# Optimization experiments

Measured on AMD Instinct MI355X. Metric: run time of the kernel, lower is better.

The kernel has to match this reference:

```python
import jax, jax.numpy as jnp
import numpy as np

N_WAY = 5
K_SHOT = 5
TEMPERATURE = 1.0
NEG = -1e9  # emulates 'column does not exist' for pad columns beyond umask_length
EPS = 1e-12  # matches torch F.normalize eps


def _l2n(x, axis):
    n = jnp.sqrt(jnp.sum(x * x, axis=axis, keepdims=True))
    return x / jnp.maximum(n, EPS)


def setup_inputs() -> dict:
    key = jax.random.key(0)
    k1, k2, k3, k4, k5 = jax.random.split(key, 5)
    b, c, h, w = 4, 64, 5, 5
    q, u = 75, 100
    support_xf = jax.random.normal(k1, (b, N_WAY * K_SHOT, c, h, w), jnp.float32)
    query_xf = jax.random.normal(k2, (b, q, c, h, w), jnp.float32)
    unlabeled_xf = jax.random.normal(k3, (b, u, c, h, w), jnp.float32)
    support_y = jax.random.randint(k4, (b, N_WAY * K_SHOT), 0, N_WAY)
    query_y = jax.random.randint(k5, (b, q), 0, N_WAY)
    return {"support_xf": support_xf, "support_y": support_y, "query_xf": query_xf,
            "query_y": query_y, "unlabeled_xf": unlabeled_xf}


def _forward(support_xf, query_xf, unlabeled_xf, query_y):
    b, q, c, h, w = query_xf.shape
    M_s = K_SHOT * h * w
    unl = unlabeled_xf.reshape(b, -1, c, h, w)
    u = unl.shape[1]
    M_u = u * h * w
    # pooled unlabeled local descriptors, flattened in (u, h, w) order -> [b, c, M_u]
    unl_feat = unl.transpose(0, 2, 1, 3, 4).reshape(b, c, M_u)
    # support -> [b, n_way, c, k_shot*h*w]
    sup = support_xf.reshape(b, N_WAY, K_SHOT, c, h, w).transpose(0, 1, 3, 2, 4, 5).reshape(b, N_WAY, c, M_s)
    # cosine similarity unlabeled -> support: [b, n_way, M_u, M_s]
    u2s = jnp.einsum('bwcn,bcm->bwmn', _l2n(sup, 2), _l2n(unl_feat, 1))
    pool = u2s.transpose(0, 2, 1, 3).reshape(b, M_u, N_WAY * M_s)
    s_nearest = jnp.argmax(pool, axis=1)          # per support loc: nearest unlabeled loc
    u_nearest = jnp.argmax(pool, axis=2)          # per unlabeled loc: nearest support loc
    mutual = jnp.take_along_axis(s_nearest, u_nearest, axis=1) == jnp.arange(M_u)[None, :]  # [b, M_u]
    # class with max similarity per unlabeled location
    cls = jnp.argmax(jnp.max(u2s, axis=-1), axis=1)  # [b, M_u]
    umask = jax.nn.one_hot(cls, N_WAY, dtype=jnp.float32).transpose(0, 2, 1) \
            * mutual[:, None, :].astype(jnp.float32)  # [b, n_way, M_u]
    counts = umask.sum(-1)                          # [b, n_way]
    L = counts.max()                                # umask_length (traced)
    # stream compaction via stable argsort of the 0/1 mask (preserves original order)
    order = jnp.argsort(-umask, axis=-1)            # jnp.argsort is stable
    pts = unl_feat.transpose(0, 2, 1)               # [b, M_u, c]
    gath = jnp.take_along_axis(pts[:, None, :, :], order[..., None], axis=2)  # [b, n_way, M_u, c]
    valid = (jnp.arange(M_u)[None, None, :] < counts[:, :, None]).astype(jnp.float32)
    comp = gath * valid[..., None]                  # rows beyond count are zeros (as in torch)
    s_cat = jnp.concatenate([sup, comp.transpose(0, 1, 3, 2)], axis=-1)  # [b, n_way, c, M_s+M_u]
    M_tot = M_s + M_u
    qn = _l2n(query_xf.reshape(b, q, c, h * w), 2)
    scn = _l2n(s_cat, 2)
    sim = jnp.einsum('bqcm,bwcn->bqwmn', qn, scn)   # [b, q, n_way, M_q, M_tot]
    sim = (sim + 1.0) * 0.5                          # FourLayer_64F branch
    # columns beyond umask_length don't exist in the torch dense tensor -> exclude from maxes
    pad = jnp.arange(M_tot)[None, None, None, None, :] >= (M_s + L)
    sim = jnp.where(pad, NEG, sim)
    M_q = h * w
    qm = sim.transpose(0, 1, 3, 2, 4).reshape(b, q, M_q, N_WAY * M_tot)
    support_nearest = jnp.argmax(qm, axis=2)        # [b, q, n_way*M_tot]
    query_nearest = jnp.argmax(qm, axis=3)          # [b, q, M_q]
    g = jnp.take_along_axis(support_nearest, query_nearest, axis=2)
    q_mask = (g == jnp.arange(M_q)[None, None, :]).astype(sim.dtype)  # mutual NN mask
    query_value = (jnp.max(sim, axis=-1) * q_mask[:, :, None, :]).sum(-1)  # [b, q, n_way]
    logits = query_value.reshape(b * q, N_WAY) / TEMPERATURE
    y = query_y.reshape(b * q)
    logp = jax.nn.log_softmax(logits, axis=-1)
    loss = -jnp.take_along_axis(logp, y[:, None], axis=1).mean()
    return loss


def reference(support_xf, support_y, query_xf, query_y, unlabeled_xf):
    return _forward(support_xf, query_xf, unlabeled_xf, query_y)
```

## Files before the change

### kernel.cpp

```cpp
#include <hip/hip_runtime.h>

#define NEGINF (-1e30f)

constexpr size_t OF_UNL  = 0;
constexpr size_t OF_SUP  = OF_UNL  + (size_t)4*2500*64;
constexpr size_t OF_SUPT = OF_SUP  + (size_t)4*5*125*64;
constexpr size_t OF_QT   = OF_SUPT + (size_t)4*5*64*128;
constexpr size_t OF_ROWV = OF_QT   + (size_t)300*28*64;
constexpr size_t OF_ROWI = OF_ROWV + (size_t)4*5*8*2500;
constexpr size_t OF_CVI  = OF_ROWI + (size_t)4*5*8*2500;
constexpr size_t OF_CMP  = OF_CVI  + (size_t)4*5*125*20*2;
constexpr size_t OF_CNT  = OF_CMP  + (size_t)4*5*2500;
constexpr size_t OF_UNEAR= OF_CNT  + 20;
constexpr size_t OF_SNEAR= OF_UNEAR+ 10000;
constexpr size_t OF_BV   = OF_SNEAR+ 2500;
constexpr size_t OF_BP   = OF_BV   + 37500;
constexpr size_t OF_AMX  = OF_BP   + 37500;

typedef __attribute__((ext_vector_type(4)))  float f4s;
typedef __attribute__((ext_vector_type(16))) float f16s;

__global__ __launch_bounds__(256) void knorm(
    const float* __restrict__ sup, const float* __restrict__ qry,
    const float* __restrict__ unl,
    float* __restrict__ unl_n, float* __restrict__ sup_n,
    float* __restrict__ supT, float* __restrict__ qt)
{
    int gid = blockIdx.x * 256 + threadIdx.x;
    if (gid >= 320000) {
        int t = gid - 320000;
        if (t < 14400) {
            int bq = t / 48, r = t % 48;
            int row = 25 + r / 16, ch = r % 16;
            *(float4*)(qt + ((size_t)bq * 28 + row) * 64 + ch * 4) =
                make_float4(0.f, 0.f, 0.f, 0.f);
        }
        return;
    }
    int loc = gid >> 4;
    int sub = gid & 15;

    const float* src;
    float* dst1; int dstr1;
    float* dst2 = nullptr;

    if (loc < 10000) {
        int b = loc / 2500, m = loc % 2500;
        int u = m / 25, hw = m % 25;
        src  = unl + ((size_t)(b*100 + u) * 64) * 25 + hw;
        dst1 = unl_n + (size_t)loc * 64; dstr1 = 1;
    } else if (loc < 12500) {
        int idx = loc - 10000;
        int b = idx / 625, r = idx % 625;
        int w = r / 125,  n = r % 125;
        int shot = n / 25, hw = n % 25;
        src  = sup + ((size_t)(b*25 + w*5 + shot) * 64) * 25 + hw;
        dst1 = sup_n + (size_t)idx * 64; dstr1 = 1;
        dst2 = supT + ((size_t)(b*5 + w) * 64) * 128 + n;
    } else {
        int idx = loc - 12500;
        int bq = idx / 25, mq = idx % 25;
        src  = qry + ((size_t)bq * 64) * 25 + mq;
        dst1 = qt + ((size_t)bq * 28 + mq) * 64; dstr1 = 1;
    }

    float v[4]; float ss = 0.f;
    int c0 = sub * 4;
#pragma unroll
    for (int j = 0; j < 4; ++j) { v[j] = src[(size_t)(c0 + j) * 25]; ss += v[j] * v[j]; }
#pragma unroll
    for (int msk = 1; msk < 16; msk <<= 1) ss += __shfl_xor(ss, msk);
    float sc = 1.f / fmaxf(sqrtf(ss), 1e-12f);
#pragma unroll
    for (int j = 0; j < 4; ++j) {
        float o = v[j] * sc;
        dst1[(size_t)(c0 + j) * dstr1] = o;
        if (dst2) dst2[(size_t)(c0 + j) * 128] = o;
    }
}

#define KB2(C) { \
    f16s s0, s1; \
    asm volatile("s_load_dwordx16 %0, %[b], %c[o0]\n\t" \
                 "s_load_dwordx16 %1, %[b], %c[o1]\n\t" \
                 "s_waitcnt lgkmcnt(0)" \
                 : "=s"(s0), "=s"(s1) \
                 : [b]"s"(sbp), [o0]"i"((C)*512), [o1]"i"((C)*512+512)); \
    float2 uv = *(const float2*)&uls[ml * 66 + (C)]; \
    acc[0]  = fmaf(uv.x, s0[0],  fmaf(uv.y, s1[0],  acc[0])); \
    acc[1]  = fmaf(uv.x, s0[1],  fmaf(uv.y, s1[1],  acc[1])); \
    acc[2]  = fmaf(uv.x, s0[2],  fmaf(uv.y, s1[2],  acc[2])); \
    acc[3]  = fmaf(uv.x, s0[3],  fmaf(uv.y, s1[3],  acc[3])); \
    acc[4]  = fmaf(uv.x, s0[4],  fmaf(uv.y, s1[4],  acc[4])); \
    acc[5]  = fmaf(uv.x, s0[5],  fmaf(uv.y, s1[5],  acc[5])); \
    acc[6]  = fmaf(uv.x, s0[6],  fmaf(uv.y, s1[6],  acc[6])); \
    acc[7]  = fmaf(uv.x, s0[7],  fmaf(uv.y, s1[7],  acc[7])); \
    acc[8]  = fmaf(uv.x, s0[8],  fmaf(uv.y, s1[8],  acc[8])); \
    acc[9]  = fmaf(uv.x, s0[9],  fmaf(uv.y, s1[9],  acc[9])); \
    acc[10] = fmaf(uv.x, s0[10], fmaf(uv.y, s1[10], acc[10])); \
    acc[11] = fmaf(uv.x, s0[11], fmaf(uv.y, s1[11], acc[11])); \
    acc[12] = fmaf(uv.x, s0[12], fmaf(uv.y, s1[12], acc[12])); \
    acc[13] = fmaf(uv.x, s0[13], fmaf(uv.y, s1[13], acc[13])); \
    acc[14] = fmaf(uv.x, s0[14], fmaf(uv.y, s1[14], acc[14])); \
    acc[15] = fmaf(uv.x, s0[15], fmaf(uv.y, s1[15], acc[15])); }
#define KB8(C) KB2(C) KB2((C)+2) KB2((C)+4) KB2((C)+6)

__global__ __launch_bounds__(256) void kb(
    const float* __restrict__ unl_n, const float* __restrict__ supT,
    float* __restrict__ rowv, int* __restrict__ rowi, float* __restrict__ colvi)
{
    int bid = blockIdx.x;
    int nc = bid & 3;
    int mb = (bid >> 2) % 20;
    int bw = bid / 80;
    int b  = bw / 5;
    int tid = threadIdx.x;
    int lane = tid & 63, wv = tid >> 6;

    __shared__ float uls[128 * 66];
    __shared__ float sv_[4][32];
    __shared__ int   si_[4][32];

    int m0 = mb * 128;
    int n0 = nc * 32;

    for (int i = tid; i < 128 * 16; i += 256) {
        int row = i >> 4, c4 = (i & 15) * 4;
        int m = m0 + row;
        float4 x = make_float4(0.f, 0.f, 0.f, 0.f);
        if (m < 2500) x = *(const float4*)(unl_n + ((size_t)(b * 2500 + m)) * 64 + c4);
        *(float2*)&uls[row * 66 + c4]     = make_float2(x.x, x.y);
        *(float2*)&uls[row * 66 + c4 + 2] = make_float2(x.z, x.w);
    }
    __syncthreads();

    int ml = tid & 127;
    int m  = m0 + ml;
    int nh = tid >> 7;
    int nbase = nh * 16;
    int nbu = __builtin_amdgcn_readfirstlane(nbase);
    int nn_total = (125 - n0) < 32 ? (125 - n0) : 32;
    const float* sbp = supT + ((size_t)bw * 64) * 128 + n0 + nbu;

    float acc[16];
#pragma unroll
    for (int j = 0; j < 16; ++j) acc[j] = 0.f;

    KB8(0)  KB8(8)  KB8(16) KB8(24)
    KB8(32) KB8(40) KB8(48) KB8(56)

    int nnloc = nn_total - nbase;
    nnloc = nnloc < 0 ? 0 : (nnloc > 16 ? 16 : nnloc);
    float rbv = NEGINF; int rbi = 0;
    for (int j = 0; j < nnloc; ++j)
        if (acc[j] > rbv) { rbv = acc[j]; rbi = n0 + nbase + j; }
    if (m < 2500) {
        int ck = nc * 2 + nh;
        rowv[((size_t)bw * 8 + ck) * 2500 + m] = rbv;
        rowi[((size_t)bw * 8 + ck) * 2500 + m] = rbi;
    }

#pragma unroll
    for (int j = 0; j < 16; ++j) {
        float v = (m < 2500 && (nbase + j) < nn_total) ? acc[j] : NEGINF;
        float vm = v;
#pragma unroll
        for (int s2 = 1; s2 < 64; s2 <<= 1) vm = fmaxf(vm, __shfl_xor(vm, s2));
        unsigned long long msk = __ballot(v == vm);
        int first = __ffsll((unsigned long long)msk) - 1;
        if (lane == 0) { sv_[wv][nbase + j] = vm; si_[wv][nbase + j] = m0 + (wv & 1) * 64 + first; }
    }
    __syncthreads();
    if (tid < nn_total) {
        int w0 = (tid < 16) ? 0 : 2;
        float v = sv_[w0][tid];     int vi = si_[w0][tid];
        float v2 = sv_[w0 + 1][tid]; int i2 = si_[w0 + 1][tid];
        if (v2 > v || (v2 == v && i2 < vi)) { v = v2; vi = i2; }
        float* cv = colvi + ((((size_t)bw) * 125 + (n0 + tid)) * 20 + mb) * 2;
        cv[0] = v; ((int*)cv)[1] = vi;
    }
}

__global__ __launch_bounds__(64) void kmerge(
    const float* __restrict__ rowv, const int* __restrict__ rowi,
    const float* __restrict__ colvi,
    int* __restrict__ unear, int* __restrict__ snear)
{
    int it = blockIdx.x * 64 + threadIdx.x;
    if (it < 10000) {
        int b = it / 2500, m = it % 2500;
        float bv = NEGINF; int bi = 0;
#pragma unroll
        for (int w = 0; w < 5; ++w) {
#pragma unroll
            for (int ck = 0; ck < 8; ++ck) {
                size_t o = (((size_t)(b * 5 + w)) * 8 + ck) * 2500 + m;
                float v = rowv[o];
                if (v > bv) { bv = v; bi = w * 125 + rowi[o]; }
            }
        }
        unear[it] = bi;
    } else if (it < 12500) {
        int idx = it - 10000;
        const float* p = colvi + (size_t)idx * 40;
        float bv = NEGINF; int bi = 0x7fffffff;
        for (int mb2 = 0; mb2 < 20; ++mb2) {
            float v = p[mb2 * 2]; int vi = ((const int*)p)[mb2 * 2 + 1];
            if (v > bv || (v == bv && vi < bi)) { bv = v; bi = vi; }
        }
        snear[idx] = bi;
    }
}

__global__ __launch_bounds__(256) void kcmp(
    const int* __restrict__ unear, const int* __restrict__ snear,
    int* __restrict__ cmp, int* __restrict__ cntg)
{
    int p = blockIdx.x;
    int b = p / 5, way = p % 5;
    int tid = threadIdx.x, lane = tid & 63, wv = tid >> 6;
    __shared__ unsigned long long masks[40];
    __shared__ int base[40];

    for (int ch = wv; ch < 40; ch += 4) {
        int m = ch * 64 + lane;
        bool ok = false;
        if (m < 2500) {
            int un = unear[b * 2500 + m];
            ok = (un / 125 == way) && (snear[b * 625 + un] == m);
        }
        unsigned long long msk = __ballot(ok ? 1 : 0);
        if (lane == 0) masks[ch] = msk;
    }
    __syncthreads();
    if (tid == 0) {
        int s = 0;
        for (int ch = 0; ch < 40; ++ch) { base[ch] = s; s += __popcll(masks[ch]); }
        cntg[p] = s;
    }
    __syncthreads();
    for (int ch = wv; ch < 40; ch += 4) {
        unsigned long long msk = masks[ch];
        if ((msk >> lane) & 1ull) {
            int pre = __popcll(msk & ((1ull << lane) - 1ull));
            cmp[(size_t)p * 2500 + base[ch] + pre] = ch * 64 + lane;
        }
    }
}

#define QLOAD(CG, Q0,Q1,Q2,Q3,Q4,Q5,Q6) \
  asm volatile( \
    "s_load_dwordx4 %0, %[b], %c[o0]\n\t" \
    "s_load_dwordx4 %1, %[b], %c[o1]\n\t" \
    "s_load_dwordx4 %2, %[b], %c[o2]\n\t" \
    "s_load_dwordx4 %3, %[b], %c[o3]\n\t" \
    "s_load_dwordx4 %4, %[b], %c[o4]\n\t" \
    "s_load_dwordx4 %5, %[b], %c[o5]\n\t" \
    "s_load_dwordx4 %6, %[b], %c[o6]\n\t" \
    "s_waitcnt lgkmcnt(0)" \
    : "=s"(Q0), "=s"(Q1), "=s"(Q2), "=s"(Q3), "=s"(Q4), "=s"(Q5), "=s"(Q6) \
    : [b]"s"(qbp), \
      [o0]"i"((CG)*16 + 0*256), [o1]"i"((CG)*16 + 1*256), \
      [o2]"i"((CG)*16 + 2*256), [o3]"i"((CG)*16 + 3*256), \
      [o4]"i"((CG)*16 + 4*256), [o5]"i"((CG)*16 + 5*256), \
      [o6]"i"((CG)*16 + 6*256))

#define CGSTEP(CG) { \
    f4s q0,q1,q2,q3,q4,q5,q6; \
    QLOAD(CG, q0,q1,q2,q3,q4,q5,q6); \
    float4 cl = *(const float4*)&cls[lane * 68 + (CG) * 4]; \
    acc[0]=fmaf(q0.x,cl.x,fmaf(q0.y,cl.y,fmaf(q0.z,cl.z,fmaf(q0.w,cl.w,acc[0])))); \
    acc[1]=fmaf(q1.x,cl.x,fmaf(q1.y,cl.y,fmaf(q1.z,cl.z,fmaf(q1.w,cl.w,acc[1])))); \
    acc[2]=fmaf(q2.x,cl.x,fmaf(q2.y,cl.y,fmaf(q2.z,cl.z,fmaf(q2.w,cl.w,acc[2])))); \
    acc[3]=fmaf(q3.x,cl.x,fmaf(q3.y,cl.y,fmaf(q3.z,cl.z,fmaf(q3.w,cl.w,acc[3])))); \
    acc[4]=fmaf(q4.x,cl.x,fmaf(q4.y,cl.y,fmaf(q4.z,cl.z,fmaf(q4.w,cl.w,acc[4])))); \
    acc[5]=fmaf(q5.x,cl.x,fmaf(q5.y,cl.y,fmaf(q5.z,cl.z,fmaf(q5.w,cl.w,acc[5])))); \
    acc[6]=fmaf(q6.x,cl.x,fmaf(q6.y,cl.y,fmaf(q6.z,cl.z,fmaf(q6.w,cl.w,acc[6])))); }

__global__ __launch_bounds__(256) void kc1(
    const float* __restrict__ qt, const float* __restrict__ sup_n,
    const float* __restrict__ unl_n, const int* __restrict__ cmp,
    const int* __restrict__ cntg,
    float* __restrict__ bvg, int* __restrict__ bpg,
    unsigned char* __restrict__ amaxg)
{
    int bid = blockIdx.x;
    int w = bid % 5, bq = bid / 5;
    int b = bq / 75;
    int tid = threadIdx.x;
    int lane = tid & 63;
    int wvu = __builtin_amdgcn_readfirstlane(tid >> 6);
    int pbw = b * 5 + w;

    int L = 0;
#pragma unroll
    for (int i = 0; i < 20; ++i) { int v = cntg[i]; L = L > v ? L : v; }
    int cntw = 0, wb = 0;
#pragma unroll
    for (int w2 = 0; w2 < 5; ++w2) {
        int c2 = cntg[b * 5 + w2];
        if (w2 < w) wb += 125 + c2;
        if (w2 == w) cntw = c2;
    }
    int cw = 125 + cntw;

    __shared__ float cls[64 * 68];
    __shared__ float amxv[4][64];
    __shared__ int   amxg_[4][64];
    __shared__ float redv[25];
    __shared__ int   redn[25];

    const float* qbp = qt + ((size_t)bq * 28 + wvu * 7) * 64;

    float rv[7]; int rn[7];
#pragma unroll
    for (int j = 0; j < 7; ++j) { rv[j] = NEGINF; rn[j] = 0x7fffffff; }

    int nb = (cw + 63) >> 6;

    for (int b4 = 0; b4 < nb; ++b4) {
        if (b4 > 0 && tid < 64) {
            int n = (b4 - 1) * 64 + tid;
            if (n < cw) {
                float v = amxv[0][tid]; int g = amxg_[0][tid];
#pragma unroll
                for (int g2 = 1; g2 < 4; ++g2)
                    if (amxv[g2][tid] > v) { v = amxv[g2][tid]; g = amxg_[g2][tid]; }
                amaxg[(size_t)bq * 3200 + (wb + n)] = (unsigned char)g;
            }
        }
#pragma unroll
        for (int k = 0; k < 4; ++k) {
            int i = tid + k * 256;
            int row = i >> 4, ch = i & 15;
            int n = b4 * 64 + row;
            float4 x = make_float4(0.f, 0.f, 0.f, 0.f);
            if (n < cw) {
                const float* cp;
                if (n < 125) cp = sup_n + (((size_t)pbw) * 125 + n) * 64;
                else { int m = cmp[((size_t)pbw) * 2500 + (n - 125)];
                       cp = unl_n + ((size_t)(b * 2500 + m)) * 64; }
                x = *(const float4*)(cp + ch * 4);
            }
            *(float4*)&cls[row * 68 + ch * 4] = x;
        }
        __syncthreads();

        float acc[7];
#pragma unroll
        for (int j = 0; j < 7; ++j) acc[j] = 0.f;

        CGSTEP(0);  CGSTEP(1);  CGSTEP(2);  CGSTEP(3);
        CGSTEP(4);  CGSTEP(5);  CGSTEP(6);  CGSTEP(7);
        CGSTEP(8);  CGSTEP(9);  CGSTEP(10); CGSTEP(11);
        CGSTEP(12); CGSTEP(13); CGSTEP(14); CGSTEP(15);

        bool colvalid = (b4 * 64 + lane) < cw;
        float cmax = NEGINF; int cam = 0;
#pragma unroll
        for (int j = 0; j < 7; ++j) {
            int mq = wvu * 7 + j;
            float s = (acc[j] + 1.0f) * 0.5f;
            float sm = (colvalid && mq < 25) ? s : NEGINF;
            if (sm > cmax) { cmax = sm; cam = mq; }
            float vm = sm;
#pragma unroll
            for (int t = 1; t < 64; t <<= 1) vm = fmaxf(vm, __shfl_xor(vm, t));
            unsigned long long msk = __ballot(sm == vm);
            int first = __ffsll(msk) - 1;
            if (vm > rv[j]) { rv[j] = vm; rn[j] = b4 * 64 + first; }
        }
        amxv[wvu][lane] = cmax; amxg_[wvu][lane] = cam;
        __syncthreads();
    }

    if (tid < 64) {
        int n = (nb - 1) * 64 + tid;
        if (n < cw) {
            float v = amxv[0][tid]; int g = amxg_[0][tid];
#pragma unroll
            for (int g2 = 1; g2 < 4; ++g2)
                if (amxv[g2][tid] > v) { v = amxv[g2][tid]; g = amxg_[g2][tid]; }
            amaxg[(size_t)bq * 3200 + (wb + n)] = (unsigned char)g;
        }
    }
    if (lane == 0) {
#pragma unroll
        for (int j = 0; j < 7; ++j) {
            int mq = wvu * 7 + j;
            if (mq < 25) { redv[mq] = rv[j]; redn[mq] = rn[j]; }
        }
    }
    __syncthreads();

    if (tid < 25) {
        float v = redv[tid]; int nn = redn[tid];
        int p = ((w * 2625 + nn) << 12) | (wb + nn);
        if (L > cntw) {
            int pp = ((w * 2625 + 125 + cntw) << 12) | 0xFFF;
            if (0.5f > v || (0.5f == v && pp < p)) { v = 0.5f; p = pp; }
        }
        size_t o = ((size_t)bq * 5 + w) * 25 + tid;
        bvg[o] = v; bpg[o] = p;
    }
}

__global__ __launch_bounds__(64) void kce(
    const float* __restrict__ bvg, const int* __restrict__ bpg,
    const unsigned char* __restrict__ amaxg, const int* __restrict__ qy,
    float* __restrict__ out)
{
    int bq = blockIdx.x;
    int tid = threadIdx.x;
    __shared__ float qmask[25];
    __shared__ float lg[5];
    if (tid < 25) {
        float v = NEGINF; int p = 0x7fffffff;
#pragma unroll
        for (int w = 0; w < 5; ++w) {
            size_t o = ((size_t)bq * 5 + w) * 25 + tid;
            float v2 = bvg[o]; int p2 = bpg[o];
            if (v2 > v || (v2 == v && p2 < p)) { v = v2; p = p2; }
        }
        int pos = p & 0xFFF;
        int g = (pos == 0xFFF) ? 0 : (int)amaxg[(size_t)bq * 3200 + pos];
        qmask[tid] = (g == tid) ? 1.0f : 0.0f;
    }
    __syncthreads();
    if (tid < 5) {
        float s = 0.f;
#pragma unroll
        for (int mq = 0; mq < 25; ++mq)
            s += bvg[((size_t)bq * 5 + tid) * 25 + mq] * qmask[mq];
        lg[tid] = s;
    }
    __syncthreads();
    if (tid == 0) {
        int y = qy[bq];
        float mx = lg[0];
#pragma unroll
        for (int w = 1; w < 5; ++w) mx = fmaxf(mx, lg[w]);
        float se = 0.f;
#pragma unroll
        for (int w = 0; w < 5; ++w) se += expf(lg[w] - mx);
        float loss = -(lg[y] - mx - logf(se));
        atomicAdd(out, loss * (1.0f / 300.0f));
    }
}

extern "C" void kernel_launch(void* const* d_in, const int* in_sizes, int n_in,
                              void* d_out, int out_size, void* d_ws, size_t ws_size,
                              hipStream_t stream)
{
    const float* sup = (const float*)d_in[0];
    const float* qry = (const float*)d_in[2];
    const int*   qy  = (const int*)d_in[3];
    const float* unl = (const float*)d_in[4];

    float* ws    = (float*)d_ws;
    float* unl_n = ws + OF_UNL;
    float* sup_n = ws + OF_SUP;
    float* supT  = ws + OF_SUPT;
    float* qt    = ws + OF_QT;
    float* rowv  = ws + OF_ROWV;
    int*   rowi  = (int*)(ws + OF_ROWI);
    float* colvi = ws + OF_CVI;
    int*   cmp   = (int*)(ws + OF_CMP);
    int*   cntg  = (int*)(ws + OF_CNT);
    int*   unear = (int*)(ws + OF_UNEAR);
    int*   snear = (int*)(ws + OF_SNEAR);
    float* bvg   = ws + OF_BV;
    int*   bpg   = (int*)(ws + OF_BP);
    unsigned char* amaxg = (unsigned char*)(ws + OF_AMX);

    hipMemsetAsync(d_out, 0, sizeof(float), stream);

    hipLaunchKernelGGL(knorm, dim3(1307), dim3(256), 0, stream,
                       sup, qry, unl, unl_n, sup_n, supT, qt);
    hipLaunchKernelGGL(kb, dim3(1600), dim3(256), 0, stream,
                       unl_n, supT, rowv, rowi, colvi);
    hipLaunchKernelGGL(kmerge, dim3(196), dim3(64), 0, stream,
                       rowv, rowi, colvi, unear, snear);
    hipLaunchKernelGGL(kcmp, dim3(20), dim3(256), 0, stream,
                       unear, snear, cmp, cntg);
    hipLaunchKernelGGL(kc1, dim3(1500), dim3(256), 0, stream,
                       qt, sup_n, unl_n, cmp, cntg, bvg, bpg, amaxg);
    hipLaunchKernelGGL(kce, dim3(300), dim3(64), 0, stream,
                       bvg, bpg, amaxg, qy, (float*)d_out);
}
```

Measured before the change: 180.5 us.

## Split kc1 column tiles across blocks and merge partial maxima in kce

The kc1 kernel now launches one block per (query, class, 64-column tile) rather than looping serially over up to four column tiles inside one block. Each block writes a per-tile partial row maximum and position, and kce reduces the four tiles per class before the existing mutual-nearest-neighbour and softmax logic. Workspace buffers for the partials reuse the rowv/rowi regions. This raises parallelism fourfold and removes the serial tile loop, at the cost of more blocks and some that only write sentinel values and exit early.

```diff
diff --git a/kernel.cpp b/kernel.cpp
--- a/kernel.cpp
+++ b/kernel.cpp
@@ -13,9 +13,9 @@
 constexpr size_t OF_CNT  = OF_CMP  + (size_t)4*5*2500;
 constexpr size_t OF_UNEAR= OF_CNT  + 20;
 constexpr size_t OF_SNEAR= OF_UNEAR+ 10000;
-constexpr size_t OF_BV   = OF_SNEAR+ 2500;
-constexpr size_t OF_BP   = OF_BV   + 37500;
-constexpr size_t OF_AMX  = OF_BP   + 37500;
+constexpr size_t OF_BV   = OF_ROWV;
+constexpr size_t OF_BP   = OF_ROWI;
+constexpr size_t OF_AMX  = OF_SNEAR + 2500 + 2*37500;
 
 typedef __attribute__((ext_vector_type(4)))  float f4s;
 typedef __attribute__((ext_vector_type(16))) float f16s;
@@ -285,7 +285,9 @@
     unsigned char* __restrict__ amaxg)
 {
     int bid = blockIdx.x;
-    int w = bid % 5, bq = bid / 5;
+    int bt = bid & 3;
+    int w  = (bid >> 2) % 5;
+    int bq = bid / 20;
     int b = bq / 75;
     int tid = threadIdx.x;
     int lane = tid & 63;
@@ -304,78 +306,73 @@
     }
     int cw = 125 + cntw;
 
+    size_t pb20 = ((size_t)bq * 20 + w * 4 + bt) * 25;
+    if (bt * 64 >= cw) {
+        if (tid < 25) { bvg[pb20 + tid] = NEGINF; bpg[pb20 + tid] = 0x7fffffff; }
+        return;
+    }
+
     __shared__ float cls[64 * 68];
     __shared__ float amxv[4][64];
     __shared__ int   amxg_[4][64];
-    __shared__ float redv[25];
-    __shared__ int   redn[25];
 
     const float* qbp = qt + ((size_t)bq * 28 + wvu * 7) * 64;
 
-    float rv[7]; int rn[7];
-#pragma unroll
-    for (int j = 0; j < 7; ++j) { rv[j] = NEGINF; rn[j] = 0x7fffffff; }
-
-    int nb = (cw + 63) >> 6;
-
-    for (int b4 = 0; b4 < nb; ++b4) {
-        if (b4 > 0 && tid < 64) {
-            int n = (b4 - 1) * 64 + tid;
-            if (n < cw) {
-                float v = amxv[0][tid]; int g = amxg_[0][tid];
-#pragma unroll
-                for (int g2 = 1; g2 < 4; ++g2)
-                    if (amxv[g2][tid] > v) { v = amxv[g2][tid]; g = amxg_[g2][tid]; }
-                amaxg[(size_t)bq * 3200 + (wb + n)] = (unsigned char)g;
+#pragma unroll
+    for (int k = 0; k < 4; ++k) {
+        int i = tid + k * 256;
+        int row = i >> 4, ch = i & 15;
+        int n = bt * 64 + row;
+        float4 x = make_float4(0.f, 0.f, 0.f, 0.f);
+        if (n < cw) {
+            const float* cp;
+            if (n < 125) cp = sup_n + (((size_t)pbw) * 125 + n) * 64;
+            else { int m = cmp[((size_t)pbw) * 2500 + (n - 125)];
+                   cp = unl_n + ((size_t)(b * 2500 + m)) * 64; }
+            x = *(const float4*)(cp + ch * 4);
+        }
+        *(float4*)&cls[row * 68 + ch * 4] = x;
+    }
+    __syncthreads();
+
+    float acc[7];
+#pragma unroll
+    for (int j = 0; j < 7; ++j) acc[j] = 0.f;
+
+    CGSTEP(0);  CGSTEP(1);  CGSTEP(2);  CGSTEP(3);
+    CGSTEP(4);  CGSTEP(5);  CGSTEP(6);  CGSTEP(7);
+    CGSTEP(8);  CGSTEP(9);  CGSTEP(10); CGSTEP(11);
+    CGSTEP(12); CGSTEP(13); CGSTEP(14); CGSTEP(15);
+
+    bool colvalid = (bt * 64 + lane) < cw;
+    float cmax = NEGINF; int cam = 0;
+#pragma unroll
+    for (int j = 0; j < 7; ++j) {
+        int mq = wvu * 7 + j;
+        float s = (acc[j] + 1.0f) * 0.5f;
+        float sm = (colvalid && mq < 25) ? s : NEGINF;
+        if (sm > cmax) { cmax = sm; cam = mq; }
+        float vm = sm;
+#pragma unroll
+        for (int t = 1; t < 64; t <<= 1) vm = fmaxf(vm, __shfl_xor(vm, t));
+        unsigned long long msk = __ballot(sm == vm);
+        int first = __ffsll(msk) - 1;
+        if (lane == 0 && mq < 25) {
+            int nn = bt * 64 + first;
+            float v = vm;
+            int p = ((w * 2625 + nn) << 12) | (wb + nn);
+            if (bt == 0 && L > cntw) {
+                int pp = ((w * 2625 + 125 + cntw) << 12) | 0xFFF;
+                if (0.5f > v || (0.5f == v && pp < p)) { v = 0.5f; p = pp; }
             }
-        }
-#pragma unroll
-        for (int k = 0; k < 4; ++k) {
-            int i = tid + k * 256;
-            int row = i >> 4, ch = i & 15;
-            int n = b4 * 64 + row;
-            float4 x = make_float4(0.f, 0.f, 0.f, 0.f);
-            if (n < cw) {
-                const float* cp;
-                if (n < 125) cp = sup_n + (((size_t)pbw) * 125 + n) * 64;
-                else { int m = cmp[((size_t)pbw) * 2500 + (n - 125)];
-                       cp = unl_n + ((size_t)(b * 2500 + m)) * 64; }
-                x = *(const float4*)(cp + ch * 4);
-            }
-            *(float4*)&cls[row * 68 + ch * 4] = x;
-        }
-        __syncthreads();
-
-        float acc[7];
-#pragma unroll
-        for (int j = 0; j < 7; ++j) acc[j] = 0.f;
-
-        CGSTEP(0);  CGSTEP(1);  CGSTEP(2);  CGSTEP(3);
-        CGSTEP(4);  CGSTEP(5);  CGSTEP(6);  CGSTEP(7);
-        CGSTEP(8);  CGSTEP(9);  CGSTEP(10); CGSTEP(11);
-        CGSTEP(12); CGSTEP(13); CGSTEP(14); CGSTEP(15);
-
-        bool colvalid = (b4 * 64 + lane) < cw;
-        float cmax = NEGINF; int cam = 0;
-#pragma unroll
-        for (int j = 0; j < 7; ++j) {
-            int mq = wvu * 7 + j;
-            float s = (acc[j] + 1.0f) * 0.5f;
-            float sm = (colvalid && mq < 25) ? s : NEGINF;
-            if (sm > cmax) { cmax = sm; cam = mq; }
-            float vm = sm;
-#pragma unroll
-            for (int t = 1; t < 64; t <<= 1) vm = fmaxf(vm, __shfl_xor(vm, t));
-            unsigned long long msk = __ballot(sm == vm);
-            int first = __ffsll(msk) - 1;
-            if (vm > rv[j]) { rv[j] = vm; rn[j] = b4 * 64 + first; }
-        }
-        amxv[wvu][lane] = cmax; amxg_[wvu][lane] = cam;
-        __syncthreads();
-    }
+            bvg[pb20 + mq] = v; bpg[pb20 + mq] = p;
+        }
+    }
+    amxv[wvu][lane] = cmax; amxg_[wvu][lane] = cam;
+    __syncthreads();
 
     if (tid < 64) {
-        int n = (nb - 1) * 64 + tid;
+        int n = bt * 64 + tid;
         if (n < cw) {
             float v = amxv[0][tid]; int g = amxg_[0][tid];
 #pragma unroll
@@ -383,25 +380,6 @@
                 if (amxv[g2][tid] > v) { v = amxv[g2][tid]; g = amxg_[g2][tid]; }
             amaxg[(size_t)bq * 3200 + (wb + n)] = (unsigned char)g;
         }
-    }
-    if (lane == 0) {
-#pragma unroll
-        for (int j = 0; j < 7; ++j) {
-            int mq = wvu * 7 + j;
-            if (mq < 25) { redv[mq] = rv[j]; redn[mq] = rn[j]; }
-        }
-    }
-    __syncthreads();
-
-    if (tid < 25) {
-        float v = redv[tid]; int nn = redn[tid];
-        int p = ((w * 2625 + nn) << 12) | (wb + nn);
-        if (L > cntw) {
-            int pp = ((w * 2625 + 125 + cntw) << 12) | 0xFFF;
-            if (0.5f > v || (0.5f == v && pp < p)) { v = 0.5f; p = pp; }
-        }
-        size_t o = ((size_t)bq * 5 + w) * 25 + tid;
-        bvg[o] = v; bpg[o] = p;
     }
 }
 
@@ -412,17 +390,24 @@
 {
     int bq = blockIdx.x;
     int tid = threadIdx.x;
+    __shared__ float mg[5][25];
     __shared__ float qmask[25];
     __shared__ float lg[5];
     if (tid < 25) {
-        float v = NEGINF; int p = 0x7fffffff;
+        float bestv = NEGINF; int bestp = 0x7fffffff;
 #pragma unroll
         for (int w = 0; w < 5; ++w) {
-            size_t o = ((size_t)bq * 5 + w) * 25 + tid;
-            float v2 = bvg[o]; int p2 = bpg[o];
-            if (v2 > v || (v2 == v && p2 < p)) { v = v2; p = p2; }
-        }
-        int pos = p & 0xFFF;
+            float vw = NEGINF; int pw = 0x7fffffff;
+#pragma unroll
+            for (int bt = 0; bt < 4; ++bt) {
+                size_t o = ((size_t)bq * 20 + w * 4 + bt) * 25 + tid;
+                float v2 = bvg[o]; int p2 = bpg[o];
+                if (v2 > vw || (v2 == vw && p2 < pw)) { vw = v2; pw = p2; }
+            }
+            mg[w][tid] = vw;
+            if (vw > bestv || (vw == bestv && pw < bestp)) { bestv = vw; bestp = pw; }
+        }
+        int pos = bestp & 0xFFF;
         int g = (pos == 0xFFF) ? 0 : (int)amaxg[(size_t)bq * 3200 + pos];
         qmask[tid] = (g == tid) ? 1.0f : 0.0f;
     }
@@ -431,7 +416,7 @@
         float s = 0.f;
 #pragma unroll
         for (int mq = 0; mq < 25; ++mq)
-            s += bvg[((size_t)bq * 5 + tid) * 25 + mq] * qmask[mq];
+            s += mg[tid][mq] * qmask[mq];
         lg[tid] = s;
     }
     __syncthreads();
@@ -483,7 +468,7 @@
                        rowv, rowi, colvi, unear, snear);
     hipLaunchKernelGGL(kcmp, dim3(20), dim3(256), 0, stream,
                        unear, snear, cmp, cntg);
-    hipLaunchKernelGGL(kc1, dim3(1500), dim3(256), 0, stream,
+    hipLaunchKernelGGL(kc1, dim3(6000), dim3(256), 0, stream,
                        qt, sup_n, unl_n, cmp, cntg, bvg, bpg, amaxg);
     hipLaunchKernelGGL(kce, dim3(300), dim3(64), 0, stream,
                        bvg, bpg, amaxg, qy, (float*)d_out);
```

Result: slower. 208.7 us (+15.6%).
